# Optimization experiments

Measured on AMD Instinct MI355X. Metric: run time of the kernel, lower is better.

The kernel has to match this reference:

```python
import jax, jax.numpy as jnp
import numpy as np

RES = 300          # grid resolution per axis
NC_D = 16          # density_n_comp
NC_A = 48          # app_n_comp
APP_DIM = 27       # app_dim
N = 500000         # number of ray samples

MAT_MODE = [[0, 1], [0, 2], [1, 2]]
VEC_MODE = [2, 1, 0]


def setup_inputs() -> dict:
    key = jax.random.key(0)
    k0, k1, k2, k3 = jax.random.split(key, 4)
    xyz_sampled = jax.random.uniform(k0, (N, 3), minval=-1.0, maxval=1.0, dtype=jnp.float32)
    plane_coef = 0.1 * jax.random.normal(k1, (3, NC_A + NC_D, RES, RES), dtype=jnp.float32)
    line_coef = 0.1 * jax.random.normal(k2, (3, NC_A + NC_D, RES, 1), dtype=jnp.float32)
    basis_W = jax.random.normal(k3, (APP_DIM, 3 * NC_A), dtype=jnp.float32) / np.sqrt(3 * NC_A)
    return {"xyz_sampled": xyz_sampled, "plane_coef": plane_coef,
            "line_coef": line_coef, "basis_W": basis_W}


def _grid_sample(img, x, y):
    """Bilinear grid_sample, align_corners=True, zeros padding.
    img: (C, H, W); x, y: (N,) normalized coords in [-1, 1] (x -> W, y -> H).
    Returns (C, N)."""
    C, H, W = img.shape
    ix = (x + 1.0) * 0.5 * (W - 1)
    iy = (y + 1.0) * 0.5 * (H - 1)
    x0f = jnp.floor(ix)
    y0f = jnp.floor(iy)
    wx = ix - x0f   # weight for x0+1
    wy = iy - y0f   # weight for y0+1
    x0 = x0f.astype(jnp.int32)
    y0 = y0f.astype(jnp.int32)
    out = jnp.zeros((C, x.shape[0]), img.dtype)
    for dx, wxc in ((0, 1.0 - wx), (1, wx)):
        for dy, wyc in ((0, 1.0 - wy), (1, wy)):
            xi = x0 + dx
            yi = y0 + dy
            valid = (xi >= 0) & (xi < W) & (yi >= 0) & (yi < H)
            xic = jnp.clip(xi, 0, W - 1)
            yic = jnp.clip(yi, 0, H - 1)
            w = jnp.where(valid, wxc * wyc, 0.0)
            out = out + img[:, yic, xic] * w
    return out


def reference(xyz_sampled, plane_coef, line_coef, basis_W):
    zeros = jnp.zeros((xyz_sampled.shape[0],), xyz_sampled.dtype)
    pf, lf = [], []
    for i in range(3):
        m0, m1 = MAT_MODE[i]
        # plane: grid = (x=xyz[m0] -> W, y=xyz[m1] -> H)
        pf.append(_grid_sample(plane_coef[i], xyz_sampled[:, m0], xyz_sampled[:, m1]))
        # line: grid = (x=0 -> W(=1), y=xyz[vecMode] -> H) => 1D interp along H
        lf.append(_grid_sample(line_coef[i], zeros, xyz_sampled[:, VEC_MODE[i]]))
    pf = jnp.stack(pf)  # (3, NC_A+NC_D, N)
    lf = jnp.stack(lf)  # (3, NC_A+NC_D, N)
    # compute_densityfeature: last density_n_comp channels, multiply and sum-reduce
    sigma_feature = jnp.sum(pf[:, NC_A:] * lf[:, NC_A:], axis=(0, 1))  # (N,)
    # compute_appfeature: first app_n_comp channels, multiply then basis projection
    app_feats = (pf[:, :NC_A] * lf[:, :NC_A]).reshape(3 * NC_A, -1)    # (3*NC_A, N)
    app_features = app_feats.T @ basis_W.T                              # (N, APP_DIM)
    return sigma_feature, app_features
```

## Files before the change

### kernel.cpp

```cpp
#include <hip/hip_runtime.h>
#include <hip/hip_bf16.h>

#define RES 300
#define NPLANE (RES * RES)
#define NC_A 48
#define APP_DIM 27
#define KDIM 144
#define KS 168

#define PT_TILES 1407
#define NPB2 (3 * PT_TILES)

__device__ __forceinline__ float bf_lo(unsigned int u) { return __uint_as_float(u << 16); }
__device__ __forceinline__ float bf_hi(unsigned int u) { return __uint_as_float(u & 0xffff0000u); }

__global__ __launch_bounds__(256) void prep(
    const float* __restrict__ plane, const float* __restrict__ line,
    const float* __restrict__ W,
    unsigned int* __restrict__ TpUo, unsigned int* __restrict__ TlP,
    __hip_bfloat16* __restrict__ Wg) {
  __shared__ __align__(16) unsigned int lt[64 * 65];
  const int blk = blockIdx.x;
  const int tid = threadIdx.x;

  if (blk < NPB2) {
    const int i  = blk / PT_TILES;
    const int t0 = blk - i * PT_TILES;
    const int p0 = t0 * 64;

    const int cb   = (tid >> 4) * 4;
    const int poff = (tid & 15) * 4;
    const bool ok  = (p0 + poff) < NPLANE;

    const float* src = plane + (size_t)(i * 64 + cb) * NPLANE + p0 + poff;
    float4 v0, v1, v2, v3;
    v0 = v1 = v2 = v3 = make_float4(0.f, 0.f, 0.f, 0.f);
    if (ok) {
      v0 = *(const float4*)(src);
      v1 = *(const float4*)(src + NPLANE);
      v2 = *(const float4*)(src + 2 * NPLANE);
      v3 = *(const float4*)(src + 3 * NPLANE);
    }
    const int col = (tid >> 4) * 2;
    const float* f0 = &v0.x; const float* f1 = &v1.x;
    const float* f2 = &v2.x; const float* f3 = &v3.x;
    #pragma unroll
    for (int j = 0; j < 4; ++j) {
      __hip_bfloat162 ha, hb;
      ha.x = __float2bfloat16(f0[j]);
      ha.y = __float2bfloat16(f1[j]);
      hb.x = __float2bfloat16(f2[j]);
      hb.y = __float2bfloat16(f3[j]);
      uint2 u;
      u.x = *(unsigned int*)&ha;
      u.y = *(unsigned int*)&hb;
      *(uint2*)&lt[(poff + j) * 34 + col] = u;
    }
    __syncthreads();
    #pragma unroll
    for (int pass = 0; pass < 2; ++pass) {
      int p  = (tid >> 3) + pass * 32;
      int c4 = (tid & 7) * 4;
      if (p0 + p < NPLANE) {
        uint2 a = *(const uint2*)&lt[p * 34 + c4];
        uint2 b = *(const uint2*)&lt[p * 34 + c4 + 2];
        uint4 w; w.x = a.x; w.y = a.y; w.z = b.x; w.w = b.y;
        *(uint4*)&TpUo[((size_t)(i * NPLANE + p0 + p)) * 32 + c4] = w;
      }
    }
  } else if (blk < NPB2 + 15) {
    const int b  = blk - NPB2;
    const int i  = b / 5;
    const int y0 = (b % 5) * 64;
    const int yl = tid & 63;
    const int cq = tid >> 6;
    #pragma unroll
    for (int k = 0; k < 16; ++k) {
      int c = cq * 16 + k;
      int y = y0 + yl;
      float a = 0.f, bv = 0.f;
      if (y < RES) {
        const float* row = line + (i * 64 + c) * RES;
        a  = row[y];
        bv = row[min(y + 1, RES - 1)];
      }
      __hip_bfloat162 h;
      h.x = __float2bfloat16(a);
      h.y = __float2bfloat16(bv);
      lt[yl * 65 + c] = *(unsigned int*)&h;
    }
    __syncthreads();
    #pragma unroll
    for (int k = 0; k < 16; ++k) {
      int ylc = k * 4 + cq;
      int c   = tid & 63;
      int y   = y0 + ylc;
      if (y < RES) TlP[((size_t)i * RES + y) * 64 + c] = lt[ylc * 65 + c];
    }
  } else {
    for (int idx = tid; idx < 2 * 5 * 64 * 8; idx += 256) {
      int j    = idx & 7;
      int lane = (idx >> 3) & 63;
      int kt   = (idx >> 9) % 5;
      int tile = idx / (5 * 64 * 8);
      int n = tile * 16 + (lane & 15);
      int k = kt * 32 + (lane >> 4) * 8 + j;
      float v = (n < APP_DIM && k < KDIM) ? W[n * KDIM + k] : 0.f;
      Wg[idx] = __float2bfloat16(v);
    }
  }
}

typedef __attribute__((ext_vector_type(8))) short short8;
typedef __attribute__((ext_vector_type(4))) float f32x4;

struct Gather {
  unsigned int u00[3], u01[3], u10[3], u11[3];
  uint2 ul[3];
  float w[3][5];
};

__device__ __forceinline__ void gather_it(
    const float* __restrict__ cp, const unsigned int* __restrict__ TpU,
    const unsigned int* __restrict__ TlP, int cl, int c2, Gather& g) {
  #pragma unroll
  for (int i = 0; i < 3; ++i) {
    float2 q0 = *(const float2*)&cp[i * 6];
    float2 q1 = *(const float2*)&cp[i * 6 + 2];
    float2 q2 = *(const float2*)&cp[i * 6 + 4];
    int pk   = __float_as_int(q0.x);
    int cell = pk & 0x7FFFF;
    int lidx = pk >> 19;
    int bidx = cell * 32 + cl;
    g.u00[i] = TpU[bidx];
    g.u01[i] = TpU[bidx + 32];
    g.u10[i] = TpU[bidx + RES * 32];
    g.u11[i] = TpU[bidx + RES * 32 + 32];
    g.ul[i]  = *(const uint2*)&TlP[(lidx << 6) + c2];
    g.w[i][0] = q0.y; g.w[i][1] = q1.x; g.w[i][2] = q1.y;
    g.w[i][3] = q2.x; g.w[i][4] = q2.y;
  }
}

__global__ __launch_bounds__(256, 5) void tensorf_main(
    const float* __restrict__ xyz, const unsigned int* __restrict__ TpU,
    const unsigned int* __restrict__ TlP, const __hip_bfloat16* __restrict__ Wg,
    float* __restrict__ out, int n_total) {
  __shared__ __hip_bfloat16 prod[64 * KS];
  __shared__ float cw[64 * 18];

  const int tid  = threadIdx.x;
  const int lane = tid & 63;
  const int wave = tid >> 6;
  const int n0   = blockIdx.x * 64;

  for (int j = tid; j < 64 * 12; j += 256) {
    int s = j / 12, kk = (j % 12) * 2;
    *(unsigned int*)&prod[s * KS + KDIM + kk] = 0u;
  }

  if (tid < 64) {
    int n = min(n0 + tid, n_total - 1);
    float crd[3] = {xyz[3 * n], xyz[3 * n + 1], xyz[3 * n + 2]};
    const int m0s[3] = {0, 0, 1}, m1s[3] = {1, 2, 2}, vms[3] = {2, 1, 0};
    float* c = &cw[tid * 18];
    #pragma unroll
    for (int i = 0; i < 3; ++i) {
      float ix = fminf(fmaxf((crd[m0s[i]] + 1.f) * 149.5f, 0.f), 299.f);
      float iy = fminf(fmaxf((crd[m1s[i]] + 1.f) * 149.5f, 0.f), 299.f);
      float ly = fminf(fmaxf((crd[vms[i]] + 1.f) * 149.5f, 0.f), 299.f);
      float x0f = fminf(floorf(ix), 298.f);
      float y0f = fminf(floorf(iy), 298.f);
      float l0f = fminf(floorf(ly), 298.f);
      float wx = ix - x0f, wy = iy - y0f, lwy = ly - l0f;
      int cell = i * NPLANE + (int)y0f * RES + (int)x0f;
      int lidx = i * RES + (int)l0f;
      c[i * 6 + 0] = __int_as_float(cell | (lidx << 19));
      c[i * 6 + 1] = (1.f - wx) * (1.f - wy);
      c[i * 6 + 2] = wx * (1.f - wy);
      c[i * 6 + 3] = (1.f - wx) * wy;
      c[i * 6 + 4] = wx * wy;
      c[i * 6 + 5] = lwy;
    }
  }
  __syncthreads();

  const int cl   = lane & 31;
  const int half = lane >> 5;
  const int c2   = cl * 2;

  Gather cur, nxt;
  gather_it(&cw[(wave * 16 + half) * 18], TpU, TlP, cl, c2, cur);
  #pragma unroll
  for (int it = 0; it < 8; ++it) {
    const int s = wave * 16 + it * 2 + half;
    if (it < 7)
      gather_it(&cw[(s + 2) * 18], TpU, TlP, cl, c2, nxt);

    float dsum = 0.f;
    #pragma unroll
    for (int i = 0; i < 3; ++i) {
      float pf_l = cur.w[i][0] * bf_lo(cur.u00[i]) + cur.w[i][1] * bf_lo(cur.u01[i]) +
                   cur.w[i][2] * bf_lo(cur.u10[i]) + cur.w[i][3] * bf_lo(cur.u11[i]);
      float pf_h = cur.w[i][0] * bf_hi(cur.u00[i]) + cur.w[i][1] * bf_hi(cur.u01[i]) +
                   cur.w[i][2] * bf_hi(cur.u10[i]) + cur.w[i][3] * bf_hi(cur.u11[i]);
      float lal = bf_lo(cur.ul[i].x), lbl = bf_hi(cur.ul[i].x);
      float lah = bf_lo(cur.ul[i].y), lbh = bf_hi(cur.ul[i].y);
      float lf_l = lal + cur.w[i][4] * (lbl - lal);
      float lf_h = lah + cur.w[i][4] * (lbh - lah);
      float prl = pf_l * lf_l, prh = pf_h * lf_h;
      if (cl < 24) {
        __hip_bfloat162 h;
        h.x = __float2bfloat16(prl);
        h.y = __float2bfloat16(prh);
        *(unsigned int*)&prod[s * KS + i * NC_A + c2] = *(unsigned int*)&h;
      } else {
        dsum += prl + prh;
      }
    }
    dsum += __shfl_xor(dsum, 1);
    dsum += __shfl_xor(dsum, 2);
    dsum += __shfl_xor(dsum, 4);
    int n = n0 + s;
    if (cl == 24 && n < n_total) out[n] = dsum;
    if (it < 7) cur = nxt;
  }
  __syncthreads();

  const int srow = lane & 15, quad = lane >> 4;
  f32x4 acc0 = {0.f, 0.f, 0.f, 0.f}, acc1 = {0.f, 0.f, 0.f, 0.f};
  const short* prodS = (const short*)prod;
  const short* WgS   = (const short*)Wg;
  const int arow = (wave * 16 + srow) * KS;
  #pragma unroll
  for (int kt = 0; kt < 5; ++kt) {
    short8 a  = *(const short8*)&prodS[arow + kt * 32 + quad * 8];
    short8 b0 = *(const short8*)&WgS[(kt * 64 + lane) * 8];
    short8 b1 = *(const short8*)&WgS[((5 + kt) * 64 + lane) * 8];
    acc0 = __builtin_amdgcn_mfma_f32_16x16x32_bf16(a, b0, acc0, 0, 0, 0);
    acc1 = __builtin_amdgcn_mfma_f32_16x16x32_bf16(a, b1, acc1, 0, 0, 0);
  }
  float* outApp = out + n_total;
  #pragma unroll
  for (int r = 0; r < 4; ++r) {
    int n = n0 + wave * 16 + quad * 4 + r;
    if (n < n_total) {
      outApp[(size_t)n * APP_DIM + srow] = acc0[r];
      if (srow < APP_DIM - 16)
        outApp[(size_t)n * APP_DIM + 16 + srow] = acc1[r];
    }
  }
}

extern "C" void kernel_launch(void* const* d_in, const int* in_sizes, int n_in,
                              void* d_out, int out_size, void* d_ws, size_t ws_size,
                              hipStream_t stream) {
  const float* xyz   = (const float*)d_in[0];
  const float* plane = (const float*)d_in[1];
  const float* line  = (const float*)d_in[2];
  const float* W     = (const float*)d_in[3];
  float* out = (float*)d_out;
  const int N = in_sizes[0] / 3;

  char* ws = (char*)d_ws;
  __hip_bfloat16* Tp  = (__hip_bfloat16*)ws;
  unsigned int*   TlP = (unsigned int*)(ws + 34560000);
  __hip_bfloat16* Wg  = (__hip_bfloat16*)(ws + 34560000 + 230400);

  prep<<<NPB2 + 16, 256, 0, stream>>>(plane, line, W, (unsigned int*)Tp, TlP, Wg);
  tensorf_main<<<(N + 63) / 64, 256, 0, stream>>>(
      xyz, (const unsigned int*)Tp, TlP, Wg, out, N);
}
```

Measured before the change: 227.1 us.

## Widen per-lane gathers to 4 channels and drop explicit software prefetch

Each lane now handles 4 channels (two packed bf16 pairs) instead of 2, so 16 lanes cover a sample and a wave processes 4 samples per iteration over 4 iterations instead of 2 samples over 8. The plane loads become 8-byte and the line loads 16-byte vector loads, halving the number of memory instructions. The explicit double-buffered next-iteration gather is replaced by an unroll-2 loop that leaves overlap to the compiler. The density reduction needs one fewer shuffle. The trade-off is that latency hiding now depends on compiler scheduling, and register pressure changes under the 5-block launch bound.

New measurement: 225.0 us. Within noise of the previous version (-0.9%).

```diff
diff --git a/kernel.cpp b/kernel.cpp
--- a/kernel.cpp
+++ b/kernel.cpp
@@ -113,34 +113,6 @@
 
 typedef __attribute__((ext_vector_type(8))) short short8;
 typedef __attribute__((ext_vector_type(4))) float f32x4;
-
-struct Gather {
-  unsigned int u00[3], u01[3], u10[3], u11[3];
-  uint2 ul[3];
-  float w[3][5];
-};
-
-__device__ __forceinline__ void gather_it(
-    const float* __restrict__ cp, const unsigned int* __restrict__ TpU,
-    const unsigned int* __restrict__ TlP, int cl, int c2, Gather& g) {
-  #pragma unroll
-  for (int i = 0; i < 3; ++i) {
-    float2 q0 = *(const float2*)&cp[i * 6];
-    float2 q1 = *(const float2*)&cp[i * 6 + 2];
-    float2 q2 = *(const float2*)&cp[i * 6 + 4];
-    int pk   = __float_as_int(q0.x);
-    int cell = pk & 0x7FFFF;
-    int lidx = pk >> 19;
-    int bidx = cell * 32 + cl;
-    g.u00[i] = TpU[bidx];
-    g.u01[i] = TpU[bidx + 32];
-    g.u10[i] = TpU[bidx + RES * 32];
-    g.u11[i] = TpU[bidx + RES * 32 + 32];
-    g.ul[i]  = *(const uint2*)&TlP[(lidx << 6) + c2];
-    g.w[i][0] = q0.y; g.w[i][1] = q1.x; g.w[i][2] = q1.y;
-    g.w[i][3] = q2.x; g.w[i][4] = q2.y;
-  }
-}
 
 __global__ __launch_bounds__(256, 5) void tensorf_main(
     const float* __restrict__ xyz, const unsigned int* __restrict__ TpU,
@@ -185,45 +157,84 @@
   }
   __syncthreads();
 
-  const int cl   = lane & 31;
-  const int half = lane >> 5;
-  const int c2   = cl * 2;
-
-  Gather cur, nxt;
-  gather_it(&cw[(wave * 16 + half) * 18], TpU, TlP, cl, c2, cur);
-  #pragma unroll
-  for (int it = 0; it < 8; ++it) {
-    const int s = wave * 16 + it * 2 + half;
-    if (it < 7)
-      gather_it(&cw[(s + 2) * 18], TpU, TlP, cl, c2, nxt);
+  const int cq = lane & 15;
+  const int sq = lane >> 4;
+  const int c4 = cq * 4;
+
+  #pragma unroll 2
+  for (int it = 0; it < 4; ++it) {
+    const int s = wave * 16 + it * 4 + sq;
+    const float* cp = &cw[s * 18];
+
+    uint2 u00[3], u01[3], u10[3], u11[3];
+    uint4 ul[3];
+    float wgt[3][5];
+    #pragma unroll
+    for (int i = 0; i < 3; ++i) {
+      float2 q0 = *(const float2*)&cp[i * 6];
+      float2 q1 = *(const float2*)&cp[i * 6 + 2];
+      float2 q2 = *(const float2*)&cp[i * 6 + 4];
+      int pk   = __float_as_int(q0.x);
+      int cell = pk & 0x7FFFF;
+      int lidx = pk >> 19;
+      int bidx = cell * 32 + cq * 2;
+      u00[i] = *(const uint2*)&TpU[bidx];
+      u01[i] = *(const uint2*)&TpU[bidx + 32];
+      u10[i] = *(const uint2*)&TpU[bidx + RES * 32];
+      u11[i] = *(const uint2*)&TpU[bidx + RES * 32 + 32];
+      ul[i]  = *(const uint4*)&TlP[(lidx << 6) + c4];
+      wgt[i][0] = q0.y; wgt[i][1] = q1.x; wgt[i][2] = q1.y;
+      wgt[i][3] = q2.x; wgt[i][4] = q2.y;
+    }
 
     float dsum = 0.f;
     #pragma unroll
     for (int i = 0; i < 3; ++i) {
-      float pf_l = cur.w[i][0] * bf_lo(cur.u00[i]) + cur.w[i][1] * bf_lo(cur.u01[i]) +
-                   cur.w[i][2] * bf_lo(cur.u10[i]) + cur.w[i][3] * bf_lo(cur.u11[i]);
-      float pf_h = cur.w[i][0] * bf_hi(cur.u00[i]) + cur.w[i][1] * bf_hi(cur.u01[i]) +
-                   cur.w[i][2] * bf_hi(cur.u10[i]) + cur.w[i][3] * bf_hi(cur.u11[i]);
-      float lal = bf_lo(cur.ul[i].x), lbl = bf_hi(cur.ul[i].x);
-      float lah = bf_lo(cur.ul[i].y), lbh = bf_hi(cur.ul[i].y);
-      float lf_l = lal + cur.w[i][4] * (lbl - lal);
-      float lf_h = lah + cur.w[i][4] * (lbh - lah);
-      float prl = pf_l * lf_l, prh = pf_h * lf_h;
-      if (cl < 24) {
-        __hip_bfloat162 h;
-        h.x = __float2bfloat16(prl);
-        h.y = __float2bfloat16(prh);
-        *(unsigned int*)&prod[s * KS + i * NC_A + c2] = *(unsigned int*)&h;
-      } else {
-        dsum += prl + prh;
+      float w00 = wgt[i][0], w01 = wgt[i][1], w10 = wgt[i][2];
+      float w11 = wgt[i][3], lw = wgt[i][4];
+      {
+        float pf_l = w00 * bf_lo(u00[i].x) + w01 * bf_lo(u01[i].x) +
+                     w10 * bf_lo(u10[i].x) + w11 * bf_lo(u11[i].x);
+        float pf_h = w00 * bf_hi(u00[i].x) + w01 * bf_hi(u01[i].x) +
+                     w10 * bf_hi(u10[i].x) + w11 * bf_hi(u11[i].x);
+        float lal = bf_lo(ul[i].x), lbl = bf_hi(ul[i].x);
+        float lah = bf_lo(ul[i].y), lbh = bf_hi(ul[i].y);
+        float lf_l = lal + lw * (lbl - lal);
+        float lf_h = lah + lw * (lbh - lah);
+        float prl = pf_l * lf_l, prh = pf_h * lf_h;
+        if (cq < 12) {
+          __hip_bfloat162 h;
+          h.x = __float2bfloat16(prl);
+          h.y = __float2bfloat16(prh);
+          *(unsigned int*)&prod[s * KS + i * NC_A + c4] = *(unsigned int*)&h;
+        } else {
+          dsum += prl + prh;
+        }
+      }
+      {
+        float pf_l = w00 * bf_lo(u00[i].y) + w01 * bf_lo(u01[i].y) +
+                     w10 * bf_lo(u10[i].y) + w11 * bf_lo(u11[i].y);
+        float pf_h = w00 * bf_hi(u00[i].y) + w01 * bf_hi(u01[i].y) +
+                     w10 * bf_hi(u10[i].y) + w11 * bf_hi(u11[i].y);
+        float lal = bf_lo(ul[i].z), lbl = bf_hi(ul[i].z);
+        float lah = bf_lo(ul[i].w), lbh = bf_hi(ul[i].w);
+        float lf_l = lal + lw * (lbl - lal);
+        float lf_h = lah + lw * (lbh - lah);
+        float prl = pf_l * lf_l, prh = pf_h * lf_h;
+        if (cq < 12) {
+          __hip_bfloat162 h;
+          h.x = __float2bfloat16(prl);
+          h.y = __float2bfloat16(prh);
+          *(unsigned int*)&prod[s * KS + i * NC_A + c4 + 2] = *(unsigned int*)&h;
+        } else {
+          dsum += prl + prh;
+        }
       }
     }
     dsum += __shfl_xor(dsum, 1);
     dsum += __shfl_xor(dsum, 2);
-    dsum += __shfl_xor(dsum, 4);
     int n = n0 + s;
-    if (cl == 24 && n < n_total) out[n] = dsum;
-    if (it < 7) cur = nxt;
+    if (cq == 12 && n < n_total) out[n] = dsum;
   }
   __syncthreads();
 
```
